# Kernel tuning notes

Measured on AMD Instinct MI355X. Metric: run time of the kernel, lower is better.

## Reference

```python
import jax, jax.numpy as jnp
import numpy as np

HIDDEN_DIM = 1024
NUM_HEADS = 16
HEAD_DIM = HIDDEN_DIM // NUM_HEADS
ROPE_BASE = 10000.0


def setup_inputs() -> dict:
    key = jax.random.key(0)
    kx, kq, kk, kv, ko = jax.random.split(key, 5)
    B, S = 2, 2048
    scale = 1.0 / np.sqrt(HIDDEN_DIM)
    x = jax.random.normal(kx, (B, S, HIDDEN_DIM), dtype=jnp.float32)
    Wq = jax.random.normal(kq, (HIDDEN_DIM, HIDDEN_DIM), dtype=jnp.float32) * scale
    Wk = jax.random.normal(kk, (HIDDEN_DIM, HIDDEN_DIM), dtype=jnp.float32) * scale
    Wv = jax.random.normal(kv, (HIDDEN_DIM, HIDDEN_DIM), dtype=jnp.float32) * scale
    Wo = jax.random.normal(ko, (HIDDEN_DIM, HIDDEN_DIM), dtype=jnp.float32) * scale
    return {"x": x, "Wq": Wq, "Wk": Wk, "Wv": Wv, "Wo": Wo}


def _apply_rope(t, positions):
    # t: (B, S, H, D), positions: (B, S)
    half = HEAD_DIM // 2
    inv_freq = 1.0 / (ROPE_BASE ** (jnp.arange(0, half, dtype=jnp.float32) * 2.0 / HEAD_DIM))
    freqs = positions[..., None].astype(jnp.float32) * inv_freq  # (B, S, D/2)
    emb = jnp.concatenate([freqs, freqs], axis=-1)  # (B, S, D)
    cos = jnp.cos(emb)[:, :, None, :]
    sin = jnp.sin(emb)[:, :, None, :]
    t1, t2 = t[..., :half], t[..., half:]
    rot = jnp.concatenate([-t2, t1], axis=-1)
    return t * cos + rot * sin


def reference(x, Wq, Wk, Wv, Wo):
    B, S, _ = x.shape
    H, D = NUM_HEADS, HEAD_DIM
    q = (x @ Wq.T).reshape(B, S, H, D)
    k = (x @ Wk.T).reshape(B, S, H, D)
    v = (x @ Wv.T).reshape(B, S, H, D)
    positions = jnp.broadcast_to(jnp.arange(S)[None, :], (B, S))
    q = _apply_rope(q, positions)
    k = _apply_rope(k, positions)
    # SDPA (non-causal, no mask): scores (B, H, S, S)
    scale = 1.0 / np.sqrt(D)
    scores = jnp.einsum('bqhd,bkhd->bhqk', q, k) * scale
    probs = jax.nn.softmax(scores, axis=-1)
    out = jnp.einsum('bhqk,bkhd->bqhd', probs, v).reshape(B, S, H * D)
    return out @ Wo.T
```

## Files before the change

kernel.cpp:

```cpp
#include <hip/hip_runtime.h>


typedef unsigned short u16;
typedef __bf16 bf16x8 __attribute__((ext_vector_type(8)));
typedef float  f32x4  __attribute__((ext_vector_type(4)));
typedef u16    u16x8  __attribute__((ext_vector_type(8)));
typedef u16    u16x4  __attribute__((ext_vector_type(4)));

#define HID 1024
#define SEQ 2048
#define NH  16
#define HD  64

__device__ __forceinline__ u16 f2bf(float f) {
  unsigned u = __float_as_uint(f);
  u += 0x7fffu + ((u >> 16) & 1u);
  return (u16)(u >> 16);
}
__device__ __forceinline__ void gl_lds16(const void* g, void* l) {
  __builtin_amdgcn_global_load_lds((const __attribute__((address_space(1))) void*)g,
                                   (__attribute__((address_space(3))) void*)l, 16, 0, 0);
}
__device__ __forceinline__ void stage_f32(const float* __restrict__ src, u16* dst) {
  float4 f0 = *(const float4*)src;
  float4 f1 = *(const float4*)(src + 4);
  u16x8 o;
  o[0] = f2bf(f0.x); o[1] = f2bf(f0.y); o[2] = f2bf(f0.z); o[3] = f2bf(f0.w);
  o[4] = f2bf(f1.x); o[5] = f2bf(f1.y); o[6] = f2bf(f1.z); o[7] = f2bf(f1.w);
  *(u16x8*)dst = o;
}
__device__ __forceinline__ int swz(int c, int r) { return c ^ (r & 7); }

__global__ void cvt_pre(const float* __restrict__ x,  const float* __restrict__ Wq,
                        const float* __restrict__ Wk, const float* __restrict__ Wv,
                        u16* __restrict__ xb, u16* __restrict__ Wqb,
                        u16* __restrict__ Wkb, u16* __restrict__ Wvb) {
  const int z = blockIdx.y;
  const float* src; u16* dst; int nchunk;
  switch (z) {
    case 0:  src = x;  dst = xb;  nchunk = 524288; break;
    case 1:  src = Wq; dst = Wqb; nchunk = 131072; break;
    case 2:  src = Wk; dst = Wkb; nchunk = 131072; break;
    default: src = Wv; dst = Wvb; nchunk = 131072; break;
  }
  const int i = blockIdx.x * 256 + threadIdx.x;
  if (i >= nchunk) return;
  stage_f32(src + (size_t)i * 8, dst + (size_t)i * 8);
}
__global__ void cvt_wo(const float* __restrict__ Wo, u16* __restrict__ Wob) {
  const int i = blockIdx.x * 256 + threadIdx.x;
  stage_f32(Wo + (size_t)i * 8, Wob + (size_t)i * 8);
}

__device__ __forceinline__ void gemm_mainloop(const u16* __restrict__ Aptr,
                                              const u16* __restrict__ Bptr,
                                              u16* a_lds, u16* b_lds,
                                              int m0, int n0, f32x4 (&acc)[4][4]) {
  const int tid  = threadIdx.x;
  const int w    = tid >> 6;
  const int lane = tid & 63;
  const int quad = lane >> 4, l15 = lane & 15;
  const int wm = (w >> 1) * 64, wn = (w & 1) * 64;
  const int srow = lane >> 3, sc = lane & 7;

  for (int k0 = 0; k0 < HID; k0 += 64) {
#pragma unroll
    for (int i = 0; i < 4; ++i) {
      const int seg = w * 4 + i;
      const int r   = seg * 8 + srow;
      const int col = k0 + swz(sc, srow) * 8;
      gl_lds16(Aptr + (size_t)(m0 + r) * HID + col, a_lds + seg * 512);
      gl_lds16(Bptr + (size_t)(n0 + r) * HID + col, b_lds + seg * 512);
    }
    __syncthreads();
#pragma unroll
    for (int kf = 0; kf < 2; ++kf) {
      bf16x8 af[4], bfr[4];
#pragma unroll
      for (int mt = 0; mt < 4; ++mt)
        af[mt] = *(const bf16x8*)&a_lds[(wm + mt * 16 + l15) * 64 + swz(kf * 4 + quad, l15) * 8];
#pragma unroll
      for (int nt = 0; nt < 4; ++nt)
        bfr[nt] = *(const bf16x8*)&b_lds[(wn + nt * 16 + l15) * 64 + swz(kf * 4 + quad, l15) * 8];
#pragma unroll
      for (int mt = 0; mt < 4; ++mt)
#pragma unroll
        for (int nt = 0; nt < 4; ++nt)
          acc[mt][nt] = __builtin_amdgcn_mfma_f32_16x16x32_bf16(af[mt], bfr[nt], acc[mt][nt], 0, 0, 0);
    }
    __syncthreads();
  }
}

__global__ __launch_bounds__(256, 2) void qkv_gemm(const u16* __restrict__ xb,
                                                   const u16* __restrict__ Wqb,
                                                   const u16* __restrict__ Wkb,
                                                   const u16* __restrict__ Wvb,
                                                   u16* __restrict__ q, u16* __restrict__ k,
                                                   u16* __restrict__ vT) {
  __shared__ __align__(16) u16 a_lds[128 * 64];
  __shared__ __align__(16) u16 b_lds[128 * 64];
  const int z = blockIdx.z;
  const u16* W = (z == 0) ? Wqb : (z == 1) ? Wkb : Wvb;

  f32x4 acc[4][4];
#pragma unroll
  for (int i = 0; i < 4; ++i)
#pragma unroll
    for (int j = 0; j < 4; ++j) acc[i][j] = (f32x4){0.f, 0.f, 0.f, 0.f};

  const int m0 = blockIdx.y * 128, n0 = blockIdx.x * 128;
  gemm_mainloop(xb, W, a_lds, b_lds, m0, n0, acc);

  const int tid = threadIdx.x, w = tid >> 6, lane = tid & 63;
  const int quad = lane >> 4, l15 = lane & 15;
  const int wm = (w >> 1) * 64, wn = (w & 1) * 64;

  if (z != 2) {
    float fr[2];
    fr[0] = __expf(-(float)(l15)      * 0.2878231366242557f);
    fr[1] = __expf(-(float)(16 + l15) * 0.2878231366242557f);
    const float qs = (z == 0) ? 0.125f : 1.f;
#pragma unroll
    for (int mt = 0; mt < 4; ++mt)
#pragma unroll
      for (int r = 0; r < 4; ++r) {
        const int s = (m0 + wm + mt * 16 + quad * 4 + r) & 2047;
#pragma unroll
        for (int p = 0; p < 2; ++p) {
          float c, sn;
          sincosf((float)s * fr[p], &sn, &c);
          const float t1 = acc[mt][p][r], t2 = acc[mt][p + 2][r];
          acc[mt][p][r]     = (t1 * c - t2 * sn) * qs;
          acc[mt][p + 2][r] = (t2 * c + t1 * sn) * qs;
        }
      }
    u16* dst = (z == 0) ? q : k;
#pragma unroll
    for (int mt = 0; mt < 4; ++mt)
#pragma unroll
      for (int nt = 0; nt < 4; ++nt) {
        const int col = n0 + wn + nt * 16 + l15;
        const int h = col >> 6, d = col & 63;
#pragma unroll
        for (int r = 0; r < 4; ++r) {
          const int row = m0 + wm + mt * 16 + quad * 4 + r;
          const int bh  = (row >> 11) * NH + h;
          dst[((size_t)bh * SEQ + (row & 2047)) * HD + d] = f2bf(acc[mt][nt][r]);
        }
      }
  } else {
#pragma unroll
    for (int mt = 0; mt < 4; ++mt) {
      const int rowbase = m0 + wm + mt * 16 + quad * 4;
      const int b = rowbase >> 11, s0 = rowbase & 2047;
#pragma unroll
      for (int nt = 0; nt < 4; ++nt) {
        const int col = n0 + wn + nt * 16 + l15;
        const int h = col >> 6, d = col & 63;
        u16x4 o;
#pragma unroll
        for (int r = 0; r < 4; ++r) o[r] = f2bf(acc[mt][nt][r]);
        *(u16x4*)&vT[((size_t)(b * NH + h) * HD + d) * SEQ + s0] = o;
      }
    }
  }
}

__global__ __launch_bounds__(256, 3) void flash(const u16* __restrict__ q,
                                                const u16* __restrict__ k,
                                                const u16* __restrict__ vT,
                                                u16* __restrict__ attn) {
  __shared__ __align__(16) u16 ktl[2 * 4096];
  __shared__ __align__(16) u16 vtl[2 * 4096];
  __shared__ __align__(16) u16 pl[4 * 2 * 16 * 72];

  const int tid = threadIdx.x, w = tid >> 6, lane = tid & 63;
  const int quad = lane >> 4, l15 = lane & 15;
  const int srow = lane >> 3, sc = lane & 7;
  const int bh = blockIdx.y;
  const int q0 = blockIdx.x * 128;

  bf16x8 qa[2][2];
#pragma unroll
  for (int qh = 0; qh < 2; ++qh) {
    const u16* qrow = q + ((size_t)bh * SEQ + q0 + w * 32 + qh * 16 + l15) * HD + quad * 8;
    qa[qh][0] = *(const bf16x8*)qrow;
    qa[qh][1] = *(const bf16x8*)(qrow + 32);
  }

  f32x4 oacc[2][4];
#pragma unroll
  for (int qh = 0; qh < 2; ++qh)
#pragma unroll
    for (int i = 0; i < 4; ++i) oacc[qh][i] = (f32x4){0.f, 0.f, 0.f, 0.f};
  float L[2] = {0.f, 0.f};

  const u16* kbase = k  + (size_t)bh * SEQ * HD;
  const u16* vtb   = vT + (size_t)bh * HD * SEQ;

#pragma unroll
  for (int i = 0; i < 2; ++i) {
    const int seg = w * 2 + i, r = seg * 8 + srow, col = swz(sc, srow) * 8;
    gl_lds16(kbase + (size_t)r * HD + col,  &ktl[seg * 512]);
    gl_lds16(vtb   + (size_t)r * SEQ + col, &vtl[seg * 512]);
  }
  __syncthreads();

  for (int t = 0; t < 32; ++t) {
    const int t0 = t * 64, buf = t & 1;
    if (t < 31) {
#pragma unroll
      for (int i = 0; i < 2; ++i) {
        const int seg = w * 2 + i, r = seg * 8 + srow, col = swz(sc, srow) * 8;
        gl_lds16(kbase + (size_t)(t0 + 64 + r) * HD + col, &ktl[(buf ^ 1) * 4096 + seg * 512]);
        gl_lds16(vtb   + (size_t)r * SEQ + t0 + 64 + col,  &vtl[(buf ^ 1) * 4096 + seg * 512]);
      }
    }

    bf16x8 kfr[2][4], bvf[2][4];
#pragma unroll
    for (int kf = 0; kf < 2; ++kf)
#pragma unroll
      for (int nt = 0; nt < 4; ++nt) {
        kfr[kf][nt] = *(const bf16x8*)&ktl[buf * 4096 + (nt * 16 + l15) * 64 + swz(kf * 4 + quad, l15) * 8];
        bvf[kf][nt] = *(const bf16x8*)&vtl[buf * 4096 + (nt * 16 + l15) * 64 + swz(kf * 4 + quad, l15) * 8];
      }

#pragma unroll
    for (int qh = 0; qh < 2; ++qh) {
      f32x4 sv[4];
#pragma unroll
      for (int nt = 0; nt < 4; ++nt) {
        sv[nt] = (f32x4){0.f, 0.f, 0.f, 0.f};
#pragma unroll
        for (int kf = 0; kf < 2; ++kf)
          sv[nt] = __builtin_amdgcn_mfma_f32_16x16x32_bf16(kfr[kf][nt], qa[qh][kf], sv[nt], 0, 0, 0);
      }
      u16* pw = &pl[(w * 2 + qh) * 1152];
#pragma unroll
      for (int nt = 0; nt < 4; ++nt) {
        u16x4 pk;
#pragma unroll
        for (int r = 0; r < 4; ++r) {
          const float pv = __expf(sv[nt][r]);
          L[qh] += pv;
          pk[r] = f2bf(pv);
        }
        *(u16x4*)&pw[l15 * 72 + nt * 16 + quad * 4] = pk;
      }
#pragma unroll
      for (int kf = 0; kf < 2; ++kf) {
        bf16x8 ap = *(const bf16x8*)&pw[l15 * 72 + kf * 32 + quad * 8];
#pragma unroll
        for (int dt = 0; dt < 4; ++dt)
          oacc[qh][dt] = __builtin_amdgcn_mfma_f32_16x16x32_bf16(ap, bvf[kf][dt], oacc[qh][dt], 0, 0, 0);
      }
    }
    __syncthreads();
  }

#pragma unroll
  for (int qh = 0; qh < 2; ++qh) {
    L[qh] += __shfl_xor(L[qh], 16, 64);
    L[qh] += __shfl_xor(L[qh], 32, 64);
  }

  const int b = bh >> 4, h = bh & 15;
#pragma unroll
  for (int qh = 0; qh < 2; ++qh)
#pragma unroll
    for (int r = 0; r < 4; ++r) {
      const float inv = 1.f / __shfl(L[qh], quad * 4 + r, 64);
      const int row = b * SEQ + q0 + w * 32 + qh * 16 + quad * 4 + r;
#pragma unroll
      for (int dt = 0; dt < 4; ++dt)
        attn[(size_t)row * HID + h * HD + dt * 16 + l15] = f2bf(oacc[qh][dt][r] * inv);
    }
}

__global__ __launch_bounds__(256, 2) void out_gemm(const u16* __restrict__ attn,
                                                   const u16* __restrict__ Wob,
                                                   float* __restrict__ out) {
  __shared__ __align__(16) u16 a_lds[128 * 64];
  __shared__ __align__(16) u16 b_lds[128 * 64];
  f32x4 acc[4][4];
#pragma unroll
  for (int i = 0; i < 4; ++i)
#pragma unroll
    for (int j = 0; j < 4; ++j) acc[i][j] = (f32x4){0.f, 0.f, 0.f, 0.f};

  const int m0 = blockIdx.y * 128, n0 = blockIdx.x * 128;
  gemm_mainloop(attn, Wob, a_lds, b_lds, m0, n0, acc);

  const int tid = threadIdx.x, w = tid >> 6, lane = tid & 63;
  const int quad = lane >> 4, l15 = lane & 15;
  const int wm = (w >> 1) * 64, wn = (w & 1) * 64;
#pragma unroll
  for (int mt = 0; mt < 4; ++mt)
#pragma unroll
    for (int nt = 0; nt < 4; ++nt) {
      const int col = n0 + wn + nt * 16 + l15;
#pragma unroll
      for (int r = 0; r < 4; ++r) {
        const int row = m0 + wm + mt * 16 + quad * 4 + r;
        out[(size_t)row * HID + col] = acc[mt][nt][r];
      }
    }
}

extern "C" void kernel_launch(void* const* d_in, const int* in_sizes, int n_in,
                              void* d_out, int out_size, void* d_ws, size_t ws_size,
                              hipStream_t stream) {
  const float* x  = (const float*)d_in[0];
  const float* Wq = (const float*)d_in[1];
  const float* Wk = (const float*)d_in[2];
  const float* Wv = (const float*)d_in[3];
  const float* Wo = (const float*)d_in[4];
  float* out = (float*)d_out;

  char* os = (char*)d_out;
  u16* Wqb = (u16*)(os);
  u16* Wkb = (u16*)(os + (2u << 20));
  u16* Wvb = (u16*)(os + (4u << 20));
  u16* xb  = (u16*)(os + (6u << 20));

  char* ws = (char*)d_ws;
  u16* q    = (u16*)(ws);
  u16* Wob  = (u16*)(ws);
  u16* k    = (u16*)(ws + (8u << 20));
  u16* vT   = (u16*)(ws + (16u << 20));
  u16* attn = (u16*)(ws + (24u << 20));

  cvt_pre<<<dim3(2048, 4), 256, 0, stream>>>(x, Wq, Wk, Wv, xb, Wqb, Wkb, Wvb);
  qkv_gemm<<<dim3(8, 32, 3), 256, 0, stream>>>(xb, Wqb, Wkb, Wvb, q, k, vT);
  flash<<<dim3(16, 32), 256, 0, stream>>>(q, k, vT, attn);
  cvt_wo<<<dim3(512), 256, 0, stream>>>(Wo, Wob);
  out_gemm<<<dim3(8, 32), 256, 0, stream>>>(attn, Wob, out);
}
```

Baseline: 213.6 us.

## Split attention over key halves, add combine kernel, shrink out-GEMM M tile

The flash kernel now splits the key/value sequence into two halves across blockIdx.z, doubling the grid to 1024 blocks. Each half writes unnormalized outputs in bf16 and its row sums, and a new combine kernel adds the two and normalizes. The output GEMM uses 64-row tiles to double its block count, and the RoPE sincos switches to the fast intrinsic. This trades an extra kernel launch, extra bf16 rounding of partial outputs, and extra global traffic for higher occupancy and parallelism on the many-CU GPU.

New measurement: 195.5 us. 8.5% less time.

```diff
diff --git a/kernel.cpp b/kernel.cpp
--- a/kernel.cpp
+++ b/kernel.cpp
@@ -12,6 +12,7 @@
 #define NH  16
 #define HD  64
 
+__device__ __forceinline__ float bf2f(u16 u) { return __uint_as_float(((unsigned)u) << 16); }
 __device__ __forceinline__ u16 f2bf(float f) {
   unsigned u = __float_as_uint(f);
   u += 0x7fffu + ((u >> 16) & 1u);
@@ -129,7 +130,7 @@
 #pragma unroll
         for (int p = 0; p < 2; ++p) {
           float c, sn;
-          sincosf((float)s * fr[p], &sn, &c);
+          __sincosf((float)s * fr[p], &sn, &c);
           const float t1 = acc[mt][p][r], t2 = acc[mt][p + 2][r];
           acc[mt][p][r]     = (t1 * c - t2 * sn) * qs;
           acc[mt][p + 2][r] = (t2 * c + t1 * sn) * qs;
@@ -170,16 +171,20 @@
 __global__ __launch_bounds__(256, 3) void flash(const u16* __restrict__ q,
                                                 const u16* __restrict__ k,
                                                 const u16* __restrict__ vT,
-                                                u16* __restrict__ attn) {
+                                                u16* __restrict__ o0, u16* __restrict__ o1,
+                                                float* __restrict__ L0, float* __restrict__ L1) {
   __shared__ __align__(16) u16 ktl[2 * 4096];
   __shared__ __align__(16) u16 vtl[2 * 4096];
-  __shared__ __align__(16) u16 pl[4 * 2 * 16 * 72];
+  __shared__ __align__(16) u16 pl[4 * 16 * 72];
 
   const int tid = threadIdx.x, w = tid >> 6, lane = tid & 63;
   const int quad = lane >> 4, l15 = lane & 15;
   const int srow = lane >> 3, sc = lane & 7;
   const int bh = blockIdx.y;
   const int q0 = blockIdx.x * 128;
+  const int z  = blockIdx.z;
+  u16*   odst = z ? o1 : o0;
+  float* Ldst = z ? L1 : L0;
 
   bf16x8 qa[2][2];
 #pragma unroll
@@ -196,8 +201,8 @@
     for (int i = 0; i < 4; ++i) oacc[qh][i] = (f32x4){0.f, 0.f, 0.f, 0.f};
   float L[2] = {0.f, 0.f};
 
-  const u16* kbase = k  + (size_t)bh * SEQ * HD;
-  const u16* vtb   = vT + (size_t)bh * HD * SEQ;
+  const u16* kbase = k  + (size_t)bh * SEQ * HD + (size_t)z * 1024 * HD;
+  const u16* vtb   = vT + (size_t)bh * HD * SEQ + (size_t)z * 1024;
 
 #pragma unroll
   for (int i = 0; i < 2; ++i) {
@@ -207,9 +212,9 @@
   }
   __syncthreads();
 
-  for (int t = 0; t < 32; ++t) {
+  for (int t = 0; t < 16; ++t) {
     const int t0 = t * 64, buf = t & 1;
-    if (t < 31) {
+    if (t < 15) {
 #pragma unroll
       for (int i = 0; i < 2; ++i) {
         const int seg = w * 2 + i, r = seg * 8 + srow, col = swz(sc, srow) * 8;
@@ -227,6 +232,7 @@
         bvf[kf][nt] = *(const bf16x8*)&vtl[buf * 4096 + (nt * 16 + l15) * 64 + swz(kf * 4 + quad, l15) * 8];
       }
 
+    u16* pw = &pl[w * 16 * 72];
 #pragma unroll
     for (int qh = 0; qh < 2; ++qh) {
       f32x4 sv[4];
@@ -237,7 +243,6 @@
         for (int kf = 0; kf < 2; ++kf)
           sv[nt] = __builtin_amdgcn_mfma_f32_16x16x32_bf16(kfr[kf][nt], qa[qh][kf], sv[nt], 0, 0, 0);
       }
-      u16* pw = &pl[(w * 2 + qh) * 1152];
 #pragma unroll
       for (int nt = 0; nt < 4; ++nt) {
         u16x4 pk;
@@ -264,6 +269,7 @@
   for (int qh = 0; qh < 2; ++qh) {
     L[qh] += __shfl_xor(L[qh], 16, 64);
     L[qh] += __shfl_xor(L[qh], 32, 64);
+    if (quad == 0) Ldst[(size_t)bh * SEQ + q0 + w * 32 + qh * 16 + l15] = L[qh];
   }
 
   const int b = bh >> 4, h = bh & 15;
@@ -271,33 +277,79 @@
   for (int qh = 0; qh < 2; ++qh)
 #pragma unroll
     for (int r = 0; r < 4; ++r) {
-      const float inv = 1.f / __shfl(L[qh], quad * 4 + r, 64);
       const int row = b * SEQ + q0 + w * 32 + qh * 16 + quad * 4 + r;
 #pragma unroll
       for (int dt = 0; dt < 4; ++dt)
-        attn[(size_t)row * HID + h * HD + dt * 16 + l15] = f2bf(oacc[qh][dt][r] * inv);
-    }
+        odst[(size_t)row * HID + h * HD + dt * 16 + l15] = f2bf(oacc[qh][dt][r]);
+    }
+}
+
+__global__ void combine(const u16* __restrict__ o1, const float* __restrict__ L0,
+                        const float* __restrict__ L1, u16* __restrict__ attn) {
+  const size_t base = ((size_t)blockIdx.x * 256 + threadIdx.x) * 8;
+  const int row = (int)(base >> 10);
+  const int h   = ((int)base & 1023) >> 6;
+  const int bh  = (row >> 11) * NH + h;
+  const int s   = row & 2047;
+  const float inv = 1.f / (L0[(size_t)bh * SEQ + s] + L1[(size_t)bh * SEQ + s]);
+  u16x8 a = *(const u16x8*)&attn[base];
+  u16x8 b = *(const u16x8*)&o1[base];
+  u16x8 o;
+#pragma unroll
+  for (int j = 0; j < 8; ++j) o[j] = f2bf((bf2f(a[j]) + bf2f(b[j])) * inv);
+  *(u16x8*)&attn[base] = o;
 }
 
 __global__ __launch_bounds__(256, 2) void out_gemm(const u16* __restrict__ attn,
                                                    const u16* __restrict__ Wob,
                                                    float* __restrict__ out) {
-  __shared__ __align__(16) u16 a_lds[128 * 64];
+  __shared__ __align__(16) u16 a_lds[64 * 64];
   __shared__ __align__(16) u16 b_lds[128 * 64];
-  f32x4 acc[4][4];
-#pragma unroll
-  for (int i = 0; i < 4; ++i)
-#pragma unroll
-    for (int j = 0; j < 4; ++j) acc[i][j] = (f32x4){0.f, 0.f, 0.f, 0.f};
-
-  const int m0 = blockIdx.y * 128, n0 = blockIdx.x * 128;
-  gemm_mainloop(attn, Wob, a_lds, b_lds, m0, n0, acc);
-
   const int tid = threadIdx.x, w = tid >> 6, lane = tid & 63;
   const int quad = lane >> 4, l15 = lane & 15;
-  const int wm = (w >> 1) * 64, wn = (w & 1) * 64;
-#pragma unroll
-  for (int mt = 0; mt < 4; ++mt)
+  const int wm = (w >> 1) * 32, wn = (w & 1) * 64;
+  const int srow = lane >> 3, sc = lane & 7;
+
+  f32x4 acc[2][4];
+#pragma unroll
+  for (int i = 0; i < 2; ++i)
+#pragma unroll
+    for (int j = 0; j < 4; ++j) acc[i][j] = (f32x4){0.f, 0.f, 0.f, 0.f};
+
+  const int m0 = blockIdx.y * 64, n0 = blockIdx.x * 128;
+
+  for (int k0 = 0; k0 < HID; k0 += 64) {
+#pragma unroll
+    for (int i = 0; i < 2; ++i) {
+      const int seg = w * 2 + i, r = seg * 8 + srow;
+      gl_lds16(attn + (size_t)(m0 + r) * HID + k0 + swz(sc, srow) * 8, a_lds + seg * 512);
+    }
+#pragma unroll
+    for (int i = 0; i < 4; ++i) {
+      const int seg = w * 4 + i, r = seg * 8 + srow;
+      gl_lds16(Wob + (size_t)(n0 + r) * HID + k0 + swz(sc, srow) * 8, b_lds + seg * 512);
+    }
+    __syncthreads();
+#pragma unroll
+    for (int kf = 0; kf < 2; ++kf) {
+      bf16x8 af[2], bfr[4];
+#pragma unroll
+      for (int mt = 0; mt < 2; ++mt)
+        af[mt] = *(const bf16x8*)&a_lds[(wm + mt * 16 + l15) * 64 + swz(kf * 4 + quad, l15) * 8];
+#pragma unroll
+      for (int nt = 0; nt < 4; ++nt)
+        bfr[nt] = *(const bf16x8*)&b_lds[(wn + nt * 16 + l15) * 64 + swz(kf * 4 + quad, l15) * 8];
+#pragma unroll
+      for (int mt = 0; mt < 2; ++mt)
+#pragma unroll
+        for (int nt = 0; nt < 4; ++nt)
+          acc[mt][nt] = __builtin_amdgcn_mfma_f32_16x16x32_bf16(af[mt], bfr[nt], acc[mt][nt], 0, 0, 0);
+    }
+    __syncthreads();
+  }
+
+#pragma unroll
+  for (int mt = 0; mt < 2; ++mt)
 #pragma unroll
     for (int nt = 0; nt < 4; ++nt) {
       const int col = n0 + wn + nt * 16 + l15;
@@ -324,6 +376,9 @@
   u16* Wkb = (u16*)(os + (2u << 20));
   u16* Wvb = (u16*)(os + (4u << 20));
   u16* xb  = (u16*)(os + (6u << 20));
+  u16*   o1 = (u16*)(os);
+  float* L0 = (float*)(os + (8u << 20));
+  float* L1 = (float*)(os + (8u << 20) + (256u << 10));
 
   char* ws = (char*)d_ws;
   u16* q    = (u16*)(ws);
@@ -334,7 +389,8 @@
 
   cvt_pre<<<dim3(2048, 4), 256, 0, stream>>>(x, Wq, Wk, Wv, xb, Wqb, Wkb, Wvb);
   qkv_gemm<<<dim3(8, 32, 3), 256, 0, stream>>>(xb, Wqb, Wkb, Wvb, q, k, vT);
-  flash<<<dim3(16, 32), 256, 0, stream>>>(q, k, vT, attn);
+  flash<<<dim3(16, 32, 2), 256, 0, stream>>>(q, k, vT, attn, o1, L0, L1);
   cvt_wo<<<dim3(512), 256, 0, stream>>>(Wo, Wob);
-  out_gemm<<<dim3(8, 32), 256, 0, stream>>>(attn, Wob, out);
-}
+  combine<<<dim3(2048), 256, 0, stream>>>(o1, L0, L1, attn);
+  out_gemm<<<dim3(8, 64), 256, 0, stream>>>(attn, Wob, out);
+}
```
